# Kernel optimization log

Measured on AMD Instinct MI355X. Metric: run time of the kernel, lower is better.

The kernel has to match this reference:

```python
import jax, jax.numpy as jnp
import numpy as np

B, T, C, D = 16, 4096, 1024, 64  # batch, tokens, d_model, head dim (d_model // n_heads)


def setup_inputs() -> dict:
    key = jax.random.key(0)
    kx, kq, kk, kv = jax.random.split(key, 4)
    scale_w = 1.0 / np.sqrt(C)
    return {
        "x": jax.random.normal(kx, (B, T, C), dtype=jnp.float32),
        "Wq": jax.random.normal(kq, (C, D), dtype=jnp.float32) * scale_w,
        "Wk": jax.random.normal(kk, (C, D), dtype=jnp.float32) * scale_w,
        "Wv": jax.random.normal(kv, (C, D), dtype=jnp.float32) * scale_w,
    }


def reference(x, Wq, Wk, Wv):
    # q, k, v: [B, T, D]; bias-free linear projections
    q = jnp.einsum("btc,cd->btd", x, Wq)
    k = jnp.einsum("btc,cd->btd", x, Wk)
    v = jnp.einsum("btc,cd->btd", x, Wv)
    # scores scaled by C**-0.5 (full d_model, matching the original module)
    scale = jnp.asarray(C, x.dtype) ** -0.5
    wei = jnp.einsum("bqd,bkd->bqk", q, k) * scale  # [B, T, T]
    wei = jax.nn.softmax(wei, axis=-1)
    # dropout is identity in eval mode
    return jnp.einsum("bqk,bkd->bqd", wei, v)  # [B, T, D]
```

## Files before the change

### kernel.cpp

```cpp
#include <hip/hip_runtime.h>
#include <stdint.h>

#define B_ 16
#define T_ 4096
#define C_ 1024
#define D_ 64
#define LOG2E 1.4426950408889634f

using f32x4 = __attribute__((ext_vector_type(4))) float;
using f32x16 = __attribute__((ext_vector_type(16))) float;
using bf16x8 = __attribute__((ext_vector_type(8))) short;
union U8 { uint32_t u[4]; bf16x8 v; };

__device__ __forceinline__ unsigned short f2bf(float x) {
  union { float f; uint32_t u; } v; v.f = x;
  uint32_t r = (v.u + 0x7fffu + ((v.u >> 16) & 1u)) >> 16;
  return (unsigned short)r;
}

__device__ __forceinline__ uint32_t cvtpk(float lo, float hi) {
  uint32_t r;
  asm("v_cvt_pk_bf16_f32 %0, %1, %2" : "=v"(r) : "v"(lo), "v"(hi));
  return r;
}

__device__ __forceinline__ void plswap(uint32_t& a, uint32_t& b) {
  asm volatile("v_permlane32_swap_b32 %0, %1" : "+v"(a), "+v"(b));
}

__device__ __forceinline__ void gload16(const void* gptr, void* lptr) {
  auto g = (const __attribute__((address_space(1))) uint32_t*)(uintptr_t)gptr;
  auto l = (__attribute__((address_space(3))) uint32_t*)(uintptr_t)lptr;
  __builtin_amdgcn_global_load_lds(g, l, 16, 0, 0);
}

#define SYNC_VM4()  asm volatile("s_waitcnt vmcnt(4)\ns_barrier" ::: "memory")
#define SYNC_VM0()  asm volatile("s_waitcnt vmcnt(0)\ns_barrier" ::: "memory")
#define SYNC_LGKM() asm volatile("s_waitcnt lgkmcnt(0)\ns_barrier" ::: "memory")

__global__ void k_prep(const float* __restrict__ Wq, const float* __restrict__ Wk,
                       const float* __restrict__ Wv, unsigned short* __restrict__ Wt) {
  int idx = blockIdx.x * 256 + threadIdx.x;
  int n = idx >> 10, k = idx & 1023;
  const float* W = (n < 64) ? Wq : (n < 128 ? Wk : Wv);
  Wt[idx] = f2bf(W[(size_t)k * 64 + (n & 63)]);
}

__global__ __launch_bounds__(256) void k_proj(const float* __restrict__ X,
                                              const unsigned short* __restrict__ Wt,
                                              unsigned short* __restrict__ Qo,
                                              unsigned short* __restrict__ Ko,
                                              unsigned short* __restrict__ Vto) {
  __shared__ float Xs[128 * 32];
  __shared__ unsigned short Ws[192 * 32];
  const int tid = threadIdx.x;
  const int wave = tid >> 6, lane = tid & 63;
  const int g = lane >> 4, c = lane & 15;
  const int m0 = blockIdx.x * 128;

  f32x4 acc[2][12];
#pragma unroll
  for (int a = 0; a < 2; ++a)
#pragma unroll
    for (int b2 = 0; b2 < 12; ++b2) acc[a][b2] = f32x4{0.f, 0.f, 0.f, 0.f};

  const int xrow = tid >> 3, xseg = tid & 7;
  const int wrow = tid >> 2, wseg = tid & 3;

  for (int step = 0; step < 32; ++step) {
    const int k0 = step * 32;
#pragma unroll
    for (int p = 0; p < 4; ++p) {
      int row = p * 32 + xrow;
      int seg = xseg ^ (row & 7);
      gload16(X + (size_t)(m0 + row) * C_ + k0 + seg * 4,
              (char*)Xs + p * 4096 + wave * 1024);
    }
#pragma unroll
    for (int p = 0; p < 3; ++p) {
      int n = p * 64 + wrow;
      int seg = wseg ^ ((n >> 1) & 3);
      gload16(Wt + (size_t)n * C_ + k0 + seg * 8,
              (char*)Ws + p * 4096 + wave * 1024);
    }
    __syncthreads();

    bf16x8 af[2];
#pragma unroll
    for (int mi = 0; mi < 2; ++mi) {
      int row = wave * 32 + mi * 16 + c;
      int sub = g * 2;
      f32x4 x0 = *(const f32x4*)((const char*)Xs + row * 128 + (((sub) ^ (row & 7)) * 16));
      f32x4 x1 = *(const f32x4*)((const char*)Xs + row * 128 + (((sub + 1) ^ (row & 7)) * 16));
      bf16x8 t;
      t[0] = (short)f2bf(x0[0]); t[1] = (short)f2bf(x0[1]);
      t[2] = (short)f2bf(x0[2]); t[3] = (short)f2bf(x0[3]);
      t[4] = (short)f2bf(x1[0]); t[5] = (short)f2bf(x1[1]);
      t[6] = (short)f2bf(x1[2]); t[7] = (short)f2bf(x1[3]);
      af[mi] = t;
    }
#pragma unroll
    for (int ni = 0; ni < 12; ++ni) {
      int n = ni * 16 + c;
      bf16x8 bf = *(const bf16x8*)((const char*)Ws + n * 64 + ((g ^ ((n >> 1) & 3)) * 16));
      acc[0][ni] = __builtin_amdgcn_mfma_f32_16x16x32_bf16(af[0], bf, acc[0][ni], 0, 0, 0);
      acc[1][ni] = __builtin_amdgcn_mfma_f32_16x16x32_bf16(af[1], bf, acc[1][ni], 0, 0, 0);
    }
    __syncthreads();
  }

  const int b = m0 >> 12;
#pragma unroll
  for (int mi = 0; mi < 2; ++mi) {
    int r0 = m0 + wave * 32 + mi * 16 + g * 4;
#pragma unroll
    for (int ni = 0; ni < 12; ++ni) {
      int col = ni * 16 + c;
      if (ni < 4) {
#pragma unroll
        for (int i = 0; i < 4; ++i)
          Qo[(size_t)(r0 + i) * D_ + col] = f2bf(acc[mi][ni][i] * (0.03125f * LOG2E));
      } else if (ni < 8) {
        int d = col - 64;
#pragma unroll
        for (int i = 0; i < 4; ++i)
          Ko[(size_t)(r0 + i) * D_ + d] = f2bf(acc[mi][ni][i]);
      } else {
        int d = col - 128;
        int tt = r0 & (T_ - 1);
        ushort4 pk;
        pk.x = f2bf(acc[mi][ni][0]); pk.y = f2bf(acc[mi][ni][1]);
        pk.z = f2bf(acc[mi][ni][2]); pk.w = f2bf(acc[mi][ni][3]);
        *(ushort4*)(Vto + (size_t)b * (D_ * T_) + (size_t)d * T_ + tt) = pk;
      }
    }
  }
}

__global__ __launch_bounds__(256, 2) void k_attn(const unsigned short* __restrict__ Qi,
                                                 const unsigned short* __restrict__ Ki,
                                                 const unsigned short* __restrict__ Vti,
                                                 float* __restrict__ Out) {
  __shared__ unsigned short Ks[2][64 * 64];
  __shared__ unsigned short Vs[2][64 * 64];

  const int tid = threadIdx.x;
  const int wave = tid >> 6, lane = tid & 63;
  const int ql = lane & 31;
  const int hi = lane >> 5;
  const int b = blockIdx.y;
  const int qb = blockIdx.x * 128 + wave * 32;

  const unsigned short* Qb = Qi + (size_t)b * T_ * D_;
  const unsigned short* Kb = Ki + (size_t)b * T_ * D_;
  const unsigned short* Vb = Vti + (size_t)b * D_ * T_;

  bf16x8 qf[4];
#pragma unroll
  for (int ks = 0; ks < 4; ++ks)
    qf[ks] = *(const bf16x8*)(Qb + (size_t)(qb + ql) * D_ + ks * 16 + 8 * hi);

  bf16x8 ones;
#pragma unroll
  for (int i = 0; i < 8; ++i) ones[i] = (short)0x3F80;

  f32x16 o0, o1, l4;
#pragma unroll
  for (int i = 0; i < 16; ++i) { o0[i] = 0.f; o1[i] = 0.f; l4[i] = 0.f; }

  const int srow = tid >> 3, sseg = tid & 7;

#define STAGE(BUF, KT)                                                          \
  do {                                                                          \
    _Pragma("unroll") for (int p = 0; p < 2; ++p) {                             \
      int row = p * 32 + srow;                                                  \
      int seg = sseg ^ (row & 7);                                               \
      gload16(Kb + (size_t)((KT) * 64 + row) * D_ + seg * 8,                    \
              (char*)&Ks[BUF][0] + p * 4096 + wave * 1024);                     \
      gload16(Vb + (size_t)row * T_ + (KT) * 64 + seg * 8,                      \
              (char*)&Vs[BUF][0] + p * 4096 + wave * 1024);                     \
    }                                                                           \
  } while (0)

#define PACK_TB(SC, PB_EVEN, PB_ODD)                                            \
  do {                                                                          \
    float p_[16];                                                               \
    _Pragma("unroll") for (int r = 0; r < 16; ++r) p_[r] = exp2f((SC)[r]);      \
    uint32_t w00 = cvtpk(p_[0], p_[1]),   w01 = cvtpk(p_[2], p_[3]);            \
    uint32_t w10 = cvtpk(p_[4], p_[5]),   w11 = cvtpk(p_[6], p_[7]);            \
    uint32_t w20 = cvtpk(p_[8], p_[9]),   w21 = cvtpk(p_[10], p_[11]);          \
    uint32_t w30 = cvtpk(p_[12], p_[13]), w31 = cvtpk(p_[14], p_[15]);          \
    plswap(w00, w10); plswap(w01, w11);                                         \
    plswap(w20, w30); plswap(w21, w31);                                         \
    { U8 t_; t_.u[0] = w00; t_.u[1] = w01; t_.u[2] = w10; t_.u[3] = w11;        \
      PB_EVEN = t_.v; }                                                         \
    { U8 t_; t_.u[0] = w20; t_.u[1] = w21; t_.u[2] = w30; t_.u[3] = w31;        \
      PB_ODD = t_.v; }                                                          \
  } while (0)

#define TILE_COMPUTE(CUR)                                                       \
  do {                                                                          \
    f32x16 s0, s1;                                                              \
    _Pragma("unroll") for (int i = 0; i < 16; ++i) { s0[i] = 0.f; s1[i] = 0.f; }\
    __builtin_amdgcn_s_setprio(1);                                              \
    _Pragma("unroll") for (int ks = 0; ks < 4; ++ks) {                          \
      int sg = ((2 * ks + hi) ^ (ql & 7)) * 16;                                 \
      bf16x8 kf0 = *(const bf16x8*)((const char*)&Ks[CUR][0] + ql * 128 + sg);  \
      bf16x8 kf1 = *(const bf16x8*)((const char*)&Ks[CUR][0] + (32 + ql) * 128 + sg); \
      s0 = __builtin_amdgcn_mfma_f32_32x32x16_bf16(kf0, qf[ks], s0, 0, 0, 0);   \
      s1 = __builtin_amdgcn_mfma_f32_32x32x16_bf16(kf1, qf[ks], s1, 0, 0, 0);   \
    }                                                                           \
    __builtin_amdgcn_s_setprio(0);                                              \
    bf16x8 pb[4];                                                               \
    PACK_TB(s0, pb[0], pb[1]);                                                  \
    PACK_TB(s1, pb[2], pb[3]);                                                  \
    __builtin_amdgcn_s_setprio(1);                                              \
    _Pragma("unroll") for (int s = 0; s < 4; ++s) {                             \
      int sg = ((2 * s + hi) ^ (ql & 7)) * 16;                                  \
      bf16x8 vf0 = *(const bf16x8*)((const char*)&Vs[CUR][0] + ql * 128 + sg);  \
      bf16x8 vf1 = *(const bf16x8*)((const char*)&Vs[CUR][0] + (32 + ql) * 128 + sg); \
      o0 = __builtin_amdgcn_mfma_f32_32x32x16_bf16(vf0, pb[s], o0, 0, 0, 0);    \
      o1 = __builtin_amdgcn_mfma_f32_32x32x16_bf16(vf1, pb[s], o1, 0, 0, 0);    \
      l4 = __builtin_amdgcn_mfma_f32_32x32x16_bf16(ones, pb[s], l4, 0, 0, 0);   \
    }                                                                           \
    __builtin_amdgcn_s_setprio(0);                                              \
  } while (0)

  STAGE(0, 0);
  int cur = 0;
  for (int kt = 0; kt < 63; ++kt) {
    STAGE(cur ^ 1, kt + 1);
    SYNC_VM4();
    TILE_COMPUTE(cur);
    SYNC_LGKM();
    cur ^= 1;
  }
  SYNC_VM0();
  TILE_COMPUTE(cur);

  float inv = 1.0f / l4[0];
  float* Ob = Out + ((size_t)b * T_ + qb + ql) * D_;
#pragma unroll
  for (int rq = 0; rq < 4; ++rq) {
    f32x4 t0, t1;
#pragma unroll
    for (int i = 0; i < 4; ++i) { t0[i] = o0[4 * rq + i] * inv; t1[i] = o1[4 * rq + i] * inv; }
    *(f32x4*)(Ob + rq * 8 + hi * 4) = t0;
    *(f32x4*)(Ob + 32 + rq * 8 + hi * 4) = t1;
  }
#undef STAGE
#undef PACK_TB
#undef TILE_COMPUTE
}

extern "C" void kernel_launch(void* const* d_in, const int* in_sizes, int n_in,
                              void* d_out, int out_size, void* d_ws, size_t ws_size,
                              hipStream_t stream) {
  const float* x  = (const float*)d_in[0];
  const float* Wq = (const float*)d_in[1];
  const float* Wk = (const float*)d_in[2];
  const float* Wv = (const float*)d_in[3];
  float* out = (float*)d_out;
  char* ws = (char*)d_ws;
  unsigned short* Wt = (unsigned short*)(ws);
  unsigned short* Qb = (unsigned short*)(ws + (1u << 20));
  unsigned short* Kb = (unsigned short*)(ws + (9u << 20));
  unsigned short* Vt = (unsigned short*)(ws + (17u << 20));

  k_prep<<<768, 256, 0, stream>>>(Wq, Wk, Wv, Wt);
  k_proj<<<512, 256, 0, stream>>>(x, Wt, Qb, Kb, Vt);
  k_attn<<<dim3(T_ / 128, B_), 256, 0, stream>>>(Qb, Kb, Vt, out);
}
```

Before: 186.3 us.

## Triple-buffer K/V staging with one barrier per tile and VALU row sums

Result: faster. 157.6 us (-15.4%).

```diff
diff --git a/kernel.cpp b/kernel.cpp
--- a/kernel.cpp
+++ b/kernel.cpp
@@ -36,7 +36,6 @@
 
 #define SYNC_VM4()  asm volatile("s_waitcnt vmcnt(4)\ns_barrier" ::: "memory")
 #define SYNC_VM0()  asm volatile("s_waitcnt vmcnt(0)\ns_barrier" ::: "memory")
-#define SYNC_LGKM() asm volatile("s_waitcnt lgkmcnt(0)\ns_barrier" ::: "memory")
 
 __global__ void k_prep(const float* __restrict__ Wq, const float* __restrict__ Wk,
                        const float* __restrict__ Wv, unsigned short* __restrict__ Wt) {
@@ -141,8 +140,7 @@
                                                  const unsigned short* __restrict__ Ki,
                                                  const unsigned short* __restrict__ Vti,
                                                  float* __restrict__ Out) {
-  __shared__ unsigned short Ks[2][64 * 64];
-  __shared__ unsigned short Vs[2][64 * 64];
+  __shared__ char LDSBUF[6 * 8192];
 
   const int tid = threadIdx.x;
   const int wave = tid >> 6, lane = tid & 63;
@@ -160,32 +158,35 @@
   for (int ks = 0; ks < 4; ++ks)
     qf[ks] = *(const bf16x8*)(Qb + (size_t)(qb + ql) * D_ + ks * 16 + 8 * hi);
 
-  bf16x8 ones;
-#pragma unroll
-  for (int i = 0; i < 8; ++i) ones[i] = (short)0x3F80;
-
-  f32x16 o0, o1, l4;
-#pragma unroll
-  for (int i = 0; i < 16; ++i) { o0[i] = 0.f; o1[i] = 0.f; l4[i] = 0.f; }
+  f32x16 o0, o1;
+  float l_loc = 0.f;
+#pragma unroll
+  for (int i = 0; i < 16; ++i) { o0[i] = 0.f; o1[i] = 0.f; }
 
   const int srow = tid >> 3, sseg = tid & 7;
 
 #define STAGE(BUF, KT)                                                          \
   do {                                                                          \
+    char* kb_ = LDSBUF + (BUF) * 8192 + wave * 1024;                            \
+    char* vb_ = LDSBUF + 24576 + (BUF) * 8192 + wave * 1024;                    \
     _Pragma("unroll") for (int p = 0; p < 2; ++p) {                             \
       int row = p * 32 + srow;                                                  \
       int seg = sseg ^ (row & 7);                                               \
-      gload16(Kb + (size_t)((KT) * 64 + row) * D_ + seg * 8,                    \
-              (char*)&Ks[BUF][0] + p * 4096 + wave * 1024);                     \
-      gload16(Vb + (size_t)row * T_ + (KT) * 64 + seg * 8,                      \
-              (char*)&Vs[BUF][0] + p * 4096 + wave * 1024);                     \
+      gload16(Kb + (size_t)((KT) * 64 + row) * D_ + seg * 8, kb_ + p * 4096);   \
+      gload16(Vb + (size_t)row * T_ + (KT) * 64 + seg * 8, vb_ + p * 4096);     \
     }                                                                           \
   } while (0)
 
 #define PACK_TB(SC, PB_EVEN, PB_ODD)                                            \
   do {                                                                          \
     float p_[16];                                                               \
-    _Pragma("unroll") for (int r = 0; r < 16; ++r) p_[r] = exp2f((SC)[r]);      \
+    _Pragma("unroll") for (int r = 0; r < 16; ++r)                              \
+        p_[r] = __builtin_amdgcn_exp2f((SC)[r]);                                \
+    float a0 = (p_[0] + p_[1]) + (p_[2] + p_[3]);                               \
+    float a1 = (p_[4] + p_[5]) + (p_[6] + p_[7]);                               \
+    float a2 = (p_[8] + p_[9]) + (p_[10] + p_[11]);                             \
+    float a3 = (p_[12] + p_[13]) + (p_[14] + p_[15]);                           \
+    l_loc += (a0 + a1) + (a2 + a3);                                             \
     uint32_t w00 = cvtpk(p_[0], p_[1]),   w01 = cvtpk(p_[2], p_[3]);            \
     uint32_t w10 = cvtpk(p_[4], p_[5]),   w11 = cvtpk(p_[6], p_[7]);            \
     uint32_t w20 = cvtpk(p_[8], p_[9]),   w21 = cvtpk(p_[10], p_[11]);          \
@@ -198,15 +199,17 @@
       PB_ODD = t_.v; }                                                          \
   } while (0)
 
-#define TILE_COMPUTE(CUR)                                                       \
+#define TILE_COMPUTE(BUF)                                                       \
   do {                                                                          \
+    const char* kb_ = LDSBUF + (BUF) * 8192;                                    \
+    const char* vb_ = LDSBUF + 24576 + (BUF) * 8192;                            \
     f32x16 s0, s1;                                                              \
     _Pragma("unroll") for (int i = 0; i < 16; ++i) { s0[i] = 0.f; s1[i] = 0.f; }\
     __builtin_amdgcn_s_setprio(1);                                              \
     _Pragma("unroll") for (int ks = 0; ks < 4; ++ks) {                          \
       int sg = ((2 * ks + hi) ^ (ql & 7)) * 16;                                 \
-      bf16x8 kf0 = *(const bf16x8*)((const char*)&Ks[CUR][0] + ql * 128 + sg);  \
-      bf16x8 kf1 = *(const bf16x8*)((const char*)&Ks[CUR][0] + (32 + ql) * 128 + sg); \
+      bf16x8 kf0 = *(const bf16x8*)(kb_ + ql * 128 + sg);                       \
+      bf16x8 kf1 = *(const bf16x8*)(kb_ + (32 + ql) * 128 + sg);                \
       s0 = __builtin_amdgcn_mfma_f32_32x32x16_bf16(kf0, qf[ks], s0, 0, 0, 0);   \
       s1 = __builtin_amdgcn_mfma_f32_32x32x16_bf16(kf1, qf[ks], s1, 0, 0, 0);   \
     }                                                                           \
@@ -217,28 +220,31 @@
     __builtin_amdgcn_s_setprio(1);                                              \
     _Pragma("unroll") for (int s = 0; s < 4; ++s) {                             \
       int sg = ((2 * s + hi) ^ (ql & 7)) * 16;                                  \
-      bf16x8 vf0 = *(const bf16x8*)((const char*)&Vs[CUR][0] + ql * 128 + sg);  \
-      bf16x8 vf1 = *(const bf16x8*)((const char*)&Vs[CUR][0] + (32 + ql) * 128 + sg); \
+      bf16x8 vf0 = *(const bf16x8*)(vb_ + ql * 128 + sg);                       \
+      bf16x8 vf1 = *(const bf16x8*)(vb_ + (32 + ql) * 128 + sg);                \
       o0 = __builtin_amdgcn_mfma_f32_32x32x16_bf16(vf0, pb[s], o0, 0, 0, 0);    \
       o1 = __builtin_amdgcn_mfma_f32_32x32x16_bf16(vf1, pb[s], o1, 0, 0, 0);    \
-      l4 = __builtin_amdgcn_mfma_f32_32x32x16_bf16(ones, pb[s], l4, 0, 0, 0);   \
     }                                                                           \
     __builtin_amdgcn_s_setprio(0);                                              \
   } while (0)
 
   STAGE(0, 0);
+  STAGE(1, 1);
   int cur = 0;
-  for (int kt = 0; kt < 63; ++kt) {
-    STAGE(cur ^ 1, kt + 1);
+  for (int kt = 0; kt < 62; ++kt) {
     SYNC_VM4();
+    int nxt = cur + 2; if (nxt >= 3) nxt -= 3;
+    STAGE(nxt, kt + 2);
     TILE_COMPUTE(cur);
-    SYNC_LGKM();
-    cur ^= 1;
-  }
+    ++cur; if (cur == 3) cur = 0;
+  }
+  SYNC_VM4();
+  TILE_COMPUTE(cur);
   SYNC_VM0();
-  TILE_COMPUTE(cur);
-
-  float inv = 1.0f / l4[0];
+  TILE_COMPUTE(0);
+
+  float l_tot = l_loc + __shfl_xor(l_loc, 32);
+  float inv = 1.0f / l_tot;
   float* Ob = Out + ((size_t)b * T_ + qb + ql) * D_;
 #pragma unroll
   for (int rq = 0; rq < 4; ++rq) {
```
